# Kernel tuning notes

Hardware: AMD Instinct MI355X
Metric: run time of the kernel (lower is better)

The kernel has to match this reference:

```python
import jax, jax.numpy as jnp
import numpy as np
from jax.ops import segment_sum

N_GRAPHS, N_PER = 100, 1000
N = N_GRAPHS * N_PER
DEG = 32
E = N * DEG
RATIO = 0.8
K = int(np.ceil(RATIO * N_PER))  # 800, equal-size graphs -> fixed k
F_IN, F_MID, F_OUT = 128, 16, 256


def setup_inputs() -> dict:
    key = jax.random.key(0)
    ks = jax.random.split(key, 10)
    x = jax.random.normal(ks[0], (N, F_IN), dtype=jnp.float32)
    # intra-graph random edges
    epg = E // N_GRAPHS
    src_l = jax.random.randint(ks[1], (N_GRAPHS, epg), 0, N_PER)
    dst_l = jax.random.randint(ks[2], (N_GRAPHS, epg), 0, N_PER)
    offs = (jnp.arange(N_GRAPHS) * N_PER)[:, None]
    edge_index = jnp.stack([(src_l + offs).reshape(-1), (dst_l + offs).reshape(-1)]).astype(jnp.int32)
    batch = jnp.repeat(jnp.arange(N_GRAPHS, dtype=jnp.int32), N_PER)
    s = lambda fan: 1.0 / np.sqrt(fan)
    W1 = jax.random.normal(ks[3], (F_IN, F_MID), dtype=jnp.float32) * s(F_IN)
    b1 = jnp.zeros((F_MID,), dtype=jnp.float32)
    w_rel = jax.random.normal(ks[4], (F_MID, 1), dtype=jnp.float32) * s(F_MID)
    b_rel = jnp.zeros((1,), dtype=jnp.float32)
    w_root = jax.random.normal(ks[5], (F_MID, 1), dtype=jnp.float32) * s(F_MID)
    W2 = jax.random.normal(ks[6], (F_MID, F_OUT), dtype=jnp.float32) * s(F_MID)
    b2 = jnp.zeros((F_OUT,), dtype=jnp.float32)
    return {"x": x, "edge_index": edge_index, "batch": batch,
            "W1": W1, "b1": b1, "w_rel": w_rel, "b_rel": b_rel,
            "w_root": w_root, "W2": W2, "b2": b2}


def _gcn(x, src, dst, W, b, self_w, ew, n):
    # GCNConv with self-loops: D^{-1/2}(A+I)D^{-1/2} X W + b; masked variant
    deg = segment_sum(ew, dst, num_segments=n) + self_w
    dis = jnp.where(deg > 0, jax.lax.rsqrt(deg), 0.0)
    xw = x @ W
    coef = ew * dis[src] * dis[dst]                       # [E]
    agg = segment_sum(xw[src] * coef[:, None], dst, num_segments=n)
    agg = agg + xw * (self_w * dis * dis)[:, None]        # self-loop term
    return agg + b


def reference(x, edge_index, batch, W1, b1, w_rel, b_rel, w_root, W2, b2):
    src, dst = edge_index[0], edge_index[1]
    ones_n = jnp.ones((N,), dtype=x.dtype)
    ones_e = jnp.ones((src.shape[0],), dtype=x.dtype)
    # conv1 + relu
    h = jax.nn.relu(_gcn(x, src, dst, W1, b1, ones_n, ones_e, N))
    # SAGPooling score: GraphConv(16,1) -> tanh
    agg = segment_sum(h[src], dst, num_segments=N)
    score = jnp.tanh((agg @ w_rel + h @ w_root + b_rel)[:, 0])  # [N]
    # per-graph top-k (equal graph sizes -> fixed K), expressed as node mask
    sc2 = score.reshape(N_GRAPHS, N_PER)
    _, idx = jax.lax.top_k(sc2, K)
    mask = jnp.zeros((N_GRAPHS, N_PER), dtype=x.dtype)
    mask = mask.at[jnp.arange(N_GRAPHS)[:, None], idx].set(1.0).reshape(-1)  # [N]
    h = h * (score * mask)[:, None]                       # x[perm] * score[perm]
    em = mask[src] * mask[dst]                            # filter_adj as edge mask
    # conv2 + relu on surviving nodes only
    h2 = jax.nn.relu(_gcn(h, src, dst, W2, b2, mask, em, N)) * mask[:, None]
    # global mean pool over surviving nodes per graph
    sums = segment_sum(h2, batch, num_segments=N_GRAPHS)
    cnt = segment_sum(mask, batch, num_segments=N_GRAPHS)
    return sums / cnt[:, None]
```

## Files before the change

kernel.cpp:

```cpp
#include <hip/hip_runtime.h>
#include <math.h>

#define N_NODES 100000
#define NG 100
#define N_PER 1000
#define N_EDGES 3200000
#define EPG 32000
#define EPG4 8000
#define EPGP 35008
#define K_TOP 800
#define F_IN 128
#define F_MID 16
#define F_OUT 256
#define SENT 1000
#define NCH 8
#define CHN 128

typedef __attribute__((ext_vector_type(8))) short short8;
typedef __attribute__((ext_vector_type(4))) float floatx4;

__device__ __forceinline__ unsigned short f2bf(float x) {
    union { float f; unsigned int u; } c; c.f = x;
    unsigned int u = c.u;
    u = u + 0x7FFF + ((u >> 16) & 1);
    return (unsigned short)(u >> 16);
}
__device__ __forceinline__ void add4(float4& a, const float4 b) {
    a.x += b.x; a.y += b.y; a.z += b.z; a.w += b.w;
}
__device__ __forceinline__ unsigned int fkey(float f) {
    unsigned int u = __float_as_uint(f);
    return (u & 0x80000000u) ? ~u : (u | 0x80000000u);
}

__global__ __launch_bounds__(1024) void k_front(const float* __restrict__ x,
    const float* __restrict__ W1, const int* __restrict__ ei,
    unsigned short* __restrict__ csr, int* __restrict__ crG,
    float* __restrict__ dis1G, float* __restrict__ xw1)
{
    int b = blockIdx.x, t = threadIdx.x;
    if (b < NG) {
        __shared__ int cnts[N_PER];
        __shared__ int cur[N_PER];
        __shared__ int rs[N_PER];
        __shared__ int scan[1024];
        int g = b, ebase = g * EPG, nbase = g * N_PER;
        if (b == 0 && t < F_MID) xw1[(size_t)N_NODES * F_MID + t] = 0.f;
        const int4* dst4 = (const int4*)(ei + N_EDGES + ebase);
        const int4* src4 = (const int4*)(ei + ebase);
        if (t < N_PER) { cnts[t] = 0; cur[t] = 0; }
        __syncthreads();
        for (int i = t; i < EPG4; i += 1024) {
            int4 d = dst4[i];
            atomicAdd(&cnts[d.x - nbase], 1);
            atomicAdd(&cnts[d.y - nbase], 1);
            atomicAdd(&cnts[d.z - nbase], 1);
            atomicAdd(&cnts[d.w - nbase], 1);
        }
        __syncthreads();
        int c = (t < N_PER) ? cnts[t] : 0;
        int c4 = (c + 3) & ~3;
        scan[t] = c4;
        __syncthreads();
        for (int dd = 1; dd < 1024; dd <<= 1) {
            int v = (t >= dd) ? scan[t - dd] : 0;
            __syncthreads();
            scan[t] += v;
            __syncthreads();
        }
        int exc = scan[t] - c4;
        unsigned short* cg = csr + (size_t)g * EPGP;
        if (t < N_PER) {
            rs[t] = exc;
            crG[nbase + t] = (c << 16) | exc;
            dis1G[nbase + t] = rsqrtf((float)c + 1.0f);
            for (int q = c; q < c4; q++) cg[exc + q] = (unsigned short)SENT;
        }
        __syncthreads();
        for (int i = t; i < EPG4; i += 1024) {
            int4 d = dst4[i];
            int4 s = src4[i];
            int dl, p;
            dl = d.x - nbase; p = rs[dl] + atomicAdd(&cur[dl], 1); cg[p] = (unsigned short)(s.x - nbase);
            dl = d.y - nbase; p = rs[dl] + atomicAdd(&cur[dl], 1); cg[p] = (unsigned short)(s.y - nbase);
            dl = d.z - nbase; p = rs[dl] + atomicAdd(&cur[dl], 1); cg[p] = (unsigned short)(s.z - nbase);
            dl = d.w - nbase; p = rs[dl] + atomicAdd(&cur[dl], 1); cg[p] = (unsigned short)(s.w - nbase);
        }
    } else {
        int n = (b - NG) * 1024 + t;
        if (n >= N_NODES) return;
        const float4* xr = (const float4*)(x + (size_t)n * F_IN);
        float4 a0 = {0,0,0,0}, a1 = a0, a2 = a0, a3 = a0;
#pragma unroll 4
        for (int kk = 0; kk < 32; kk++) {
            float4 xv = xr[kk];
#pragma unroll
            for (int r = 0; r < 4; r++) {
                const float4* wr = (const float4*)(W1 + (kk * 4 + r) * F_MID);
                float xs = (r == 0) ? xv.x : (r == 1) ? xv.y : (r == 2) ? xv.z : xv.w;
                float4 w0 = wr[0], w1 = wr[1], w2 = wr[2], w3 = wr[3];
                a0.x = fmaf(xs, w0.x, a0.x); a0.y = fmaf(xs, w0.y, a0.y);
                a0.z = fmaf(xs, w0.z, a0.z); a0.w = fmaf(xs, w0.w, a0.w);
                a1.x = fmaf(xs, w1.x, a1.x); a1.y = fmaf(xs, w1.y, a1.y);
                a1.z = fmaf(xs, w1.z, a1.z); a1.w = fmaf(xs, w1.w, a1.w);
                a2.x = fmaf(xs, w2.x, a2.x); a2.y = fmaf(xs, w2.y, a2.y);
                a2.z = fmaf(xs, w2.z, a2.z); a2.w = fmaf(xs, w2.w, a2.w);
                a3.x = fmaf(xs, w3.x, a3.x); a3.y = fmaf(xs, w3.y, a3.y);
                a3.z = fmaf(xs, w3.z, a3.z); a3.w = fmaf(xs, w3.w, a3.w);
            }
        }
        float4* op = (float4*)(xw1 + (size_t)n * F_MID);
        op[0] = a0; op[1] = a1; op[2] = a2; op[3] = a3;
    }
}

__global__ __launch_bounds__(512) void k_conv1(const unsigned short* __restrict__ csr,
    const int* __restrict__ crG,
    const float* __restrict__ dis1G, const float* __restrict__ xw1,
    const float* __restrict__ b1, const float* __restrict__ w_rel,
    const float* __restrict__ w_root,
    float* __restrict__ hG, float* __restrict__ hwG, float* __restrict__ hroG)
{
    __shared__ float dis1l[N_PER + 1];
    int t = threadIdx.x, b = blockIdx.x;
    int g = b % NG, chunk = b / NG;
    int nbase = g * N_PER;
    const unsigned short* cg = csr + (size_t)g * EPGP;
    if (b == 0 && t < F_MID) hG[(size_t)N_NODES * F_MID + t] = 0.f;
    for (int i = t; i < N_PER; i += 512) dis1l[i] = dis1G[nbase + i];
    if (t == 0) dis1l[SENT] = 0.f;
    __syncthreads();

    int grp = t >> 2, l = t & 3;
    int n = chunk * CHN + grp;
    if (n >= N_PER) return;
    int cr = crG[nbase + n];
    int c4 = ((cr >> 16) + 3) & ~3;
    const unsigned short* cp = cg + (cr & 0xFFFF);
    float4 a0 = {0,0,0,0}, a1 = a0, a2 = a0, a3 = a0;
    for (int k = 0; k < c4; k += 4) {
        uint2 wv = *(const uint2*)(cp + k);
        int s0 = wv.x & 0xFFFF, s1 = wv.x >> 16, s2 = wv.y & 0xFFFF, s3 = wv.y >> 16;
        float4 v0 = *(const float4*)(xw1 + ((size_t)(nbase + s0) << 4) + 4 * l);
        float4 v1 = *(const float4*)(xw1 + ((size_t)(nbase + s1) << 4) + 4 * l);
        float4 v2 = *(const float4*)(xw1 + ((size_t)(nbase + s2) << 4) + 4 * l);
        float4 v3 = *(const float4*)(xw1 + ((size_t)(nbase + s3) << 4) + 4 * l);
        float w0 = dis1l[s0], w1 = dis1l[s1], w2 = dis1l[s2], w3 = dis1l[s3];
        a0.x = fmaf(v0.x, w0, a0.x); a0.y = fmaf(v0.y, w0, a0.y); a0.z = fmaf(v0.z, w0, a0.z); a0.w = fmaf(v0.w, w0, a0.w);
        a1.x = fmaf(v1.x, w1, a1.x); a1.y = fmaf(v1.y, w1, a1.y); a1.z = fmaf(v1.z, w1, a1.z); a1.w = fmaf(v1.w, w1, a1.w);
        a2.x = fmaf(v2.x, w2, a2.x); a2.y = fmaf(v2.y, w2, a2.y); a2.z = fmaf(v2.z, w2, a2.z); a2.w = fmaf(v2.w, w2, a2.w);
        a3.x = fmaf(v3.x, w3, a3.x); a3.y = fmaf(v3.y, w3, a3.y); a3.z = fmaf(v3.z, w3, a3.z); a3.w = fmaf(v3.w, w3, a3.w);
    }
    add4(a0, a1); add4(a2, a3); add4(a0, a2);
    float dn = dis1l[n];
    float4 sfr = *(const float4*)(xw1 + ((size_t)(nbase + n) << 4) + 4 * l);
    float4 b14 = *(const float4*)(b1 + 4 * l);
    float4 hv;
    hv.x = fmaxf(fmaf(dn, fmaf(sfr.x, dn, a0.x), b14.x), 0.f);
    hv.y = fmaxf(fmaf(dn, fmaf(sfr.y, dn, a0.y), b14.y), 0.f);
    hv.z = fmaxf(fmaf(dn, fmaf(sfr.z, dn, a0.z), b14.z), 0.f);
    hv.w = fmaxf(fmaf(dn, fmaf(sfr.w, dn, a0.w), b14.w), 0.f);
    *(float4*)(hG + ((size_t)(nbase + n) << 4) + 4 * l) = hv;

    float4 wr4 = *(const float4*)(w_rel + 4 * l);
    float4 wo4 = *(const float4*)(w_root + 4 * l);
    float p1 = hv.x * wr4.x + hv.y * wr4.y + hv.z * wr4.z + hv.w * wr4.w;
    float p2 = hv.x * wo4.x + hv.y * wo4.y + hv.z * wo4.z + hv.w * wo4.w;
    p1 += __shfl_xor(p1, 1); p1 += __shfl_xor(p1, 2);
    p2 += __shfl_xor(p2, 1); p2 += __shfl_xor(p2, 2);
    if (l == 0) { hwG[nbase + n] = p1; hroG[nbase + n] = p2; }
}

__global__ __launch_bounds__(1024) void k_mid(const unsigned short* __restrict__ csr,
    const int* __restrict__ crG,
    const float* __restrict__ hwG, const float* __restrict__ hroG,
    const float* __restrict__ b_rel,
    float* __restrict__ mskG, float* __restrict__ dis2G, float* __restrict__ wsrcG,
    float* __restrict__ out)
{
    __shared__ float hwl[N_PER + 1];
    __shared__ float sc[N_PER];
    __shared__ float msk[N_PER + 1];
    __shared__ int cntl[N_PER];
    __shared__ int rsl[N_PER];
    __shared__ int hist[1024];
    __shared__ int sh_b1, sh_r1, sh_b2, sh_r2, sh_len, sh_cntgt;
    __shared__ float sh_thr;

    int t = threadIdx.x, g = blockIdx.x;
    int nbase = g * N_PER;
    const unsigned short* cg = csr + (size_t)g * EPGP;
    int grp = t >> 2, l = t & 3;

    if (t < N_PER) {
        int cr = crG[nbase + t];
        cntl[t] = cr >> 16; rsl[t] = cr & 0xFFFF;
        hwl[t] = hwG[nbase + t];
    }
    if (t == 0) { sh_cntgt = 0; sh_len = 0; hwl[SENT] = 0.f; }
    if (t < F_OUT) out[g * F_OUT + t] = 0.f;
    float brel = b_rel[0];
    __syncthreads();

#pragma unroll
    for (int rr = 0; rr < 4; rr++) {
        int n = grp + 256 * rr;
        if (n < N_PER) {
            int c4 = (cntl[n] + 3) & ~3;
            const unsigned short* cp = cg + rsl[n];
            float sm = 0.f;
            for (int k = 0; k < c4; k += 4) {
                uint2 wv = *(const uint2*)(cp + k);
                int s = (l == 0) ? (int)(wv.x & 0xFFFF) : (l == 1) ? (int)(wv.x >> 16)
                      : (l == 2) ? (int)(wv.y & 0xFFFF) : (int)(wv.y >> 16);
                sm += hwl[s];
            }
            sm += __shfl_xor(sm, 1); sm += __shfl_xor(sm, 2);
            if (l == 0) sc[n] = tanhf(sm + hroG[nbase + n] + brel);
        }
    }
    __syncthreads();

    unsigned int mykey = (t < N_PER) ? fkey(sc[t]) : 0u;
    hist[t] = 0;
    __syncthreads();
    if (t < N_PER) atomicAdd(&hist[mykey >> 22], 1);
    __syncthreads();
    {
        int v0 = hist[t]; __syncthreads();
        hist[1023 - t] = v0; __syncthreads();
        for (int dd = 1; dd < 1024; dd <<= 1) {
            int v = (t >= dd) ? hist[t - dd] : 0;
            __syncthreads(); hist[t] += v; __syncthreads();
        }
        int Sb = hist[1023 - t];
        int Snext = (t == 1023) ? 0 : hist[1022 - t];
        if (Sb >= K_TOP && Snext < K_TOP) { sh_b1 = t; sh_r1 = K_TOP - Snext; }
    }
    __syncthreads();
    int b1v = sh_b1, r1 = sh_r1;
    hist[t] = 0;
    __syncthreads();
    if (t < N_PER && (int)(mykey >> 22) == b1v) atomicAdd(&hist[(mykey >> 12) & 1023], 1);
    __syncthreads();
    {
        int v0 = hist[t]; __syncthreads();
        hist[1023 - t] = v0; __syncthreads();
        for (int dd = 1; dd < 1024; dd <<= 1) {
            int v = (t >= dd) ? hist[t - dd] : 0;
            __syncthreads(); hist[t] += v; __syncthreads();
        }
        int Sb = hist[1023 - t];
        int Snext = (t == 1023) ? 0 : hist[1022 - t];
        if (Sb >= r1 && Snext < r1) { sh_b2 = t; sh_r2 = r1 - Snext; }
    }
    __syncthreads();
    unsigned int pref = ((unsigned int)b1v << 10) | (unsigned int)sh_b2;
    int r2 = sh_r2;
    __syncthreads();
    if (t < N_PER && (mykey >> 12) == pref) { int p = atomicAdd(&sh_len, 1); hist[p] = (int)mykey; }
    __syncthreads();
    {
        int L = sh_len;
        if (t < L) {
            unsigned int k0 = (unsigned int)hist[t];
            int gcnt = 0, ecnt = 0;
            for (int q2 = 0; q2 < L; q2++) {
                unsigned int kq = (unsigned int)hist[q2];
                gcnt += (kq > k0); ecnt += (kq == k0);
            }
            if (gcnt < r2 && r2 <= gcnt + ecnt)
                sh_thr = __uint_as_float((k0 & 0x80000000u) ? (k0 & 0x7FFFFFFFu) : ~k0);
        }
    }
    __syncthreads();
    float thr = sh_thr;

    {
        bool pred = (t < N_PER) && (sc[t] > thr);
        unsigned long long bal = __ballot(pred);
        if ((t & 63) == 0) atomicAdd(&sh_cntgt, (int)__popcll(bal));
    }
    __syncthreads();
    {
        int need = K_TOP - sh_cntgt;
        if (t < N_PER) {
            float v = sc[t];
            float mm;
            if (v > thr) mm = 1.f;
            else if (v < thr) mm = 0.f;
            else {
                int r = 0;
                for (int q2 = 0; q2 < t; q2++) if (sc[q2] == thr) r++;
                mm = (r < need) ? 1.f : 0.f;
            }
            msk[t] = mm;
        }
        if (t == 0) msk[SENT] = 0.f;
    }
    __syncthreads();

#pragma unroll
    for (int rr = 0; rr < 4; rr++) {
        int n = grp + 256 * rr;
        if (n < N_PER) {
            int c4 = (cntl[n] + 3) & ~3;
            const unsigned short* cp = cg + rsl[n];
            float sm = 0.f;
            for (int k = 0; k < c4; k += 4) {
                uint2 wv = *(const uint2*)(cp + k);
                int s = (l == 0) ? (int)(wv.x & 0xFFFF) : (l == 1) ? (int)(wv.x >> 16)
                      : (l == 2) ? (int)(wv.y & 0xFFFF) : (int)(wv.y >> 16);
                sm += msk[s];
            }
            sm += __shfl_xor(sm, 1); sm += __shfl_xor(sm, 2);
            if (l == 0) {
                float d2 = msk[n] * (sm + 1.f);
                float di = (d2 > 0.f) ? rsqrtf(d2) : 0.f;
                mskG[nbase + n] = msk[n];
                dis2G[nbase + n] = di;
                wsrcG[nbase + n] = sc[n] * msk[n] * di;
            }
        }
    }
}

__global__ __launch_bounds__(512) void k_conv2(const unsigned short* __restrict__ csr,
    const int* __restrict__ crG,
    const float* __restrict__ hG, const float* __restrict__ wsrcG,
    const float* __restrict__ dis2G, const float* __restrict__ mskG,
    const float* __restrict__ W2, const float* __restrict__ b2,
    float* __restrict__ out)
{
    __shared__ float wsrcl[N_PER + 1];
    __shared__ __align__(16) unsigned short fbf[CHN * F_MID];
    __shared__ __align__(16) unsigned short w2t[F_OUT * F_MID];
    __shared__ float mskl[CHN];
    int t = threadIdx.x, b = blockIdx.x;
    int g = b % NG, chunk = b / NG;
    int nbase = g * N_PER, n0 = chunk * CHN;
    const unsigned short* cg = csr + (size_t)g * EPGP;

    for (int i = t; i < N_PER; i += 512) wsrcl[i] = wsrcG[nbase + i];
    if (t == 0) wsrcl[SENT] = 0.f;
    for (int i = t; i < F_OUT * F_MID; i += 512) {
        int f = i >> 4, jj = i & 15;
        w2t[i] = f2bf(W2[jj * F_OUT + f]);
    }
    __syncthreads();

    int grp = t >> 2, l = t & 3;
    int n = n0 + grp;
    if (n < N_PER) {
        float di = dis2G[nbase + n];
        float4 pv = {0.f, 0.f, 0.f, 0.f};
        if (di != 0.f) {
            int cr = crG[nbase + n];
            int c4 = ((cr >> 16) + 3) & ~3;
            const unsigned short* cp = cg + (cr & 0xFFFF);
            float4 a0 = {0,0,0,0}, a1 = a0, a2 = a0, a3 = a0;
            for (int k = 0; k < c4; k += 4) {
                uint2 wv = *(const uint2*)(cp + k);
                int s0 = wv.x & 0xFFFF, s1 = wv.x >> 16, s2 = wv.y & 0xFFFF, s3 = wv.y >> 16;
                float4 v0 = *(const float4*)(hG + ((size_t)(nbase + s0) << 4) + 4 * l);
                float4 v1 = *(const float4*)(hG + ((size_t)(nbase + s1) << 4) + 4 * l);
                float4 v2 = *(const float4*)(hG + ((size_t)(nbase + s2) << 4) + 4 * l);
                float4 v3 = *(const float4*)(hG + ((size_t)(nbase + s3) << 4) + 4 * l);
                float w0 = wsrcl[s0], w1 = wsrcl[s1], w2 = wsrcl[s2], w3 = wsrcl[s3];
                a0.x = fmaf(v0.x, w0, a0.x); a0.y = fmaf(v0.y, w0, a0.y); a0.z = fmaf(v0.z, w0, a0.z); a0.w = fmaf(v0.w, w0, a0.w);
                a1.x = fmaf(v1.x, w1, a1.x); a1.y = fmaf(v1.y, w1, a1.y); a1.z = fmaf(v1.z, w1, a1.z); a1.w = fmaf(v1.w, w1, a1.w);
                a2.x = fmaf(v2.x, w2, a2.x); a2.y = fmaf(v2.y, w2, a2.y); a2.z = fmaf(v2.z, w2, a2.z); a2.w = fmaf(v2.w, w2, a2.w);
                a3.x = fmaf(v3.x, w3, a3.x); a3.y = fmaf(v3.y, w3, a3.y); a3.z = fmaf(v3.z, w3, a3.z); a3.w = fmaf(v3.w, w3, a3.w);
            }
            add4(a0, a1); add4(a2, a3); add4(a0, a2);
            float wn = wsrcl[n];
            float4 hs = *(const float4*)(hG + ((size_t)(nbase + n) << 4) + 4 * l);
            pv.x = di * fmaf(hs.x, wn, a0.x);
            pv.y = di * fmaf(hs.y, wn, a0.y);
            pv.z = di * fmaf(hs.z, wn, a0.z);
            pv.w = di * fmaf(hs.w, wn, a0.w);
        }
        unsigned int pk0 = (unsigned int)f2bf(pv.x) | ((unsigned int)f2bf(pv.y) << 16);
        unsigned int pk1 = (unsigned int)f2bf(pv.z) | ((unsigned int)f2bf(pv.w) << 16);
        *(unsigned int*)(fbf + grp * F_MID + 4 * l) = pk0;
        *(unsigned int*)(fbf + grp * F_MID + 4 * l + 2) = pk1;
        if (l == 0) mskl[grp] = mskG[nbase + n];
    } else {
        *(unsigned int*)(fbf + grp * F_MID + 4 * l) = 0u;
        *(unsigned int*)(fbf + grp * F_MID + 4 * l + 2) = 0u;
        if (l == 0) mskl[grp] = 0.f;
    }
    __syncthreads();

    {
        int wave = t >> 6, lane = t & 63;
        int q = lane >> 4, fl = lane & 15;
        int c0 = 32 * wave + fl, c1 = c0 + 16;
        float b2f0 = b2[c0], b2f1 = b2[c1];
        short8 bfrag0 = {0,0,0,0,0,0,0,0}, bfrag1 = bfrag0;
        if (q < 2) {
            bfrag0 = *(const short8*)(w2t + c0 * F_MID + q * 8);
            bfrag1 = *(const short8*)(w2t + c1 * F_MID + q * 8);
        }
        floatx4 zero = {0.f, 0.f, 0.f, 0.f};
        float acc0 = 0.f, acc1 = 0.f;
        for (int tile = 0; tile < CHN / 16; tile++) {
            short8 afrag = {0,0,0,0,0,0,0,0};
            int na = tile * 16 + fl;
            if (q < 2)
                afrag = *(const short8*)(fbf + na * F_MID + q * 8);
            floatx4 d0 = __builtin_amdgcn_mfma_f32_16x16x32_bf16(afrag, bfrag0, zero, 0, 0, 0);
            floatx4 d1 = __builtin_amdgcn_mfma_f32_16x16x32_bf16(afrag, bfrag1, zero, 0, 0, 0);
#pragma unroll
            for (int r = 0; r < 4; r++) {
                int nd = tile * 16 + q * 4 + r;
                float m = mskl[nd];
                acc0 += m * fmaxf(d0[r] + b2f0, 0.f);
                acc1 += m * fmaxf(d1[r] + b2f1, 0.f);
            }
        }
        acc0 += __shfl_xor(acc0, 16); acc0 += __shfl_xor(acc0, 32);
        acc1 += __shfl_xor(acc1, 16); acc1 += __shfl_xor(acc1, 32);
        if (lane < 16) {
            atomicAdd(&out[g * F_OUT + c0], acc0 * (1.0f / (float)K_TOP));
            atomicAdd(&out[g * F_OUT + c1], acc1 * (1.0f / (float)K_TOP));
        }
    }
}

extern "C" void kernel_launch(void* const* d_in, const int* in_sizes, int n_in,
                              void* d_out, int out_size, void* d_ws, size_t ws_size,
                              hipStream_t stream) {
    const float* x      = (const float*)d_in[0];
    const int*   ei     = (const int*)d_in[1];
    const float* W1     = (const float*)d_in[3];
    const float* b1     = (const float*)d_in[4];
    const float* w_rel  = (const float*)d_in[5];
    const float* b_rel  = (const float*)d_in[6];
    const float* w_root = (const float*)d_in[7];
    const float* W2     = (const float*)d_in[8];
    const float* b2     = (const float*)d_in[9];
    float* out = (float*)d_out;

    char* ws = (char*)d_ws;
    size_t o = 0;
    auto nxt = [&](size_t bytes) { void* p = ws + o; o += (bytes + 255) & ~(size_t)255; return p; };
    unsigned short* csr = (unsigned short*)nxt((size_t)NG * EPGP * sizeof(unsigned short));
    int*   crG   = (int*)nxt((size_t)N_NODES * sizeof(int));
    float* dis1G = (float*)nxt((size_t)N_NODES * sizeof(float));
    float* xw1   = (float*)nxt(((size_t)N_NODES + 1) * F_MID * sizeof(float));
    float* hG    = (float*)nxt(((size_t)N_NODES + 1) * F_MID * sizeof(float));
    float* hwG   = (float*)nxt((size_t)N_NODES * sizeof(float));
    float* hroG  = (float*)nxt((size_t)N_NODES * sizeof(float));
    float* mskG  = (float*)nxt((size_t)N_NODES * sizeof(float));
    float* dis2G = (float*)nxt((size_t)N_NODES * sizeof(float));
    float* wsrcG = (float*)nxt((size_t)N_NODES * sizeof(float));

    int gemm_blocks = (N_NODES + 1023) / 1024;
    k_front<<<NG + gemm_blocks, 1024, 0, stream>>>(x, W1, ei, csr, crG, dis1G, xw1);
    k_conv1<<<NG * NCH, 512, 0, stream>>>(csr, crG, dis1G, xw1, b1, w_rel, w_root, hG, hwG, hroG);
    k_mid<<<NG, 1024, 0, stream>>>(csr, crG, hwG, hroG, b_rel, mskG, dis2G, wsrcG, out);
    k_conv2<<<NG * NCH, 512, 0, stream>>>(csr, crG, hG, wsrcG, dis2G, mskG, W2, b2, out);
}
```

Measured before the change: 234.7 us.

## Build per-graph CSR in shared memory using saved atomic ranks, then copy out

The CSR construction in the front kernel now keeps the slot index returned by the counting atomics, packed four 8-bit ranks per edge quad in shared memory. The scatter pass then needs no second set of atomics. The whole per-graph CSR is assembled in shared memory and written to global memory with coalesced 16-byte stores, replacing scattered 2-byte global writes. This raises shared memory use to roughly 120 KB per block, which may limit occupancy. The 8-bit ranks assume each destination has in-degree of at most 255.

New measurement: 224.7 us. -4.3%, faster.

```diff
diff --git a/kernel.cpp b/kernel.cpp
--- a/kernel.cpp
+++ b/kernel.cpp
@@ -38,24 +38,27 @@
     unsigned short* __restrict__ csr, int* __restrict__ crG,
     float* __restrict__ dis1G, float* __restrict__ xw1)
 {
+    __shared__ int cnts[N_PER];
+    __shared__ int rs[N_PER];
+    __shared__ int scan[1024];
+    __shared__ unsigned int rank4[EPG4];
+    __shared__ __align__(16) unsigned short csrl[EPGP];
+
     int b = blockIdx.x, t = threadIdx.x;
     if (b < NG) {
-        __shared__ int cnts[N_PER];
-        __shared__ int cur[N_PER];
-        __shared__ int rs[N_PER];
-        __shared__ int scan[1024];
         int g = b, ebase = g * EPG, nbase = g * N_PER;
         if (b == 0 && t < F_MID) xw1[(size_t)N_NODES * F_MID + t] = 0.f;
         const int4* dst4 = (const int4*)(ei + N_EDGES + ebase);
         const int4* src4 = (const int4*)(ei + ebase);
-        if (t < N_PER) { cnts[t] = 0; cur[t] = 0; }
+        if (t < N_PER) cnts[t] = 0;
         __syncthreads();
         for (int i = t; i < EPG4; i += 1024) {
             int4 d = dst4[i];
-            atomicAdd(&cnts[d.x - nbase], 1);
-            atomicAdd(&cnts[d.y - nbase], 1);
-            atomicAdd(&cnts[d.z - nbase], 1);
-            atomicAdd(&cnts[d.w - nbase], 1);
+            unsigned r0 = (unsigned)atomicAdd(&cnts[d.x - nbase], 1);
+            unsigned r1 = (unsigned)atomicAdd(&cnts[d.y - nbase], 1);
+            unsigned r2 = (unsigned)atomicAdd(&cnts[d.z - nbase], 1);
+            unsigned r3 = (unsigned)atomicAdd(&cnts[d.w - nbase], 1);
+            rank4[i] = r0 | (r1 << 8) | (r2 << 16) | (r3 << 24);
         }
         __syncthreads();
         int c = (t < N_PER) ? cnts[t] : 0;
@@ -69,22 +72,27 @@
             __syncthreads();
         }
         int exc = scan[t] - c4;
-        unsigned short* cg = csr + (size_t)g * EPGP;
         if (t < N_PER) {
             rs[t] = exc;
             crG[nbase + t] = (c << 16) | exc;
             dis1G[nbase + t] = rsqrtf((float)c + 1.0f);
-            for (int q = c; q < c4; q++) cg[exc + q] = (unsigned short)SENT;
+            for (int q = c; q < c4; q++) csrl[exc + q] = (unsigned short)SENT;
         }
         __syncthreads();
         for (int i = t; i < EPG4; i += 1024) {
             int4 d = dst4[i];
             int4 s = src4[i];
-            int dl, p;
-            dl = d.x - nbase; p = rs[dl] + atomicAdd(&cur[dl], 1); cg[p] = (unsigned short)(s.x - nbase);
-            dl = d.y - nbase; p = rs[dl] + atomicAdd(&cur[dl], 1); cg[p] = (unsigned short)(s.y - nbase);
-            dl = d.z - nbase; p = rs[dl] + atomicAdd(&cur[dl], 1); cg[p] = (unsigned short)(s.z - nbase);
-            dl = d.w - nbase; p = rs[dl] + atomicAdd(&cur[dl], 1); cg[p] = (unsigned short)(s.w - nbase);
+            unsigned rk = rank4[i];
+            csrl[rs[d.x - nbase] + (rk & 255u)]         = (unsigned short)(s.x - nbase);
+            csrl[rs[d.y - nbase] + ((rk >> 8) & 255u)]  = (unsigned short)(s.y - nbase);
+            csrl[rs[d.z - nbase] + ((rk >> 16) & 255u)] = (unsigned short)(s.z - nbase);
+            csrl[rs[d.w - nbase] + (rk >> 24)]          = (unsigned short)(s.w - nbase);
+        }
+        __syncthreads();
+        {
+            const uint4* sv = (const uint4*)csrl;
+            uint4* dv = (uint4*)(csr + (size_t)g * EPGP);
+            for (int i = t; i < EPGP / 8; i += 1024) dv[i] = sv[i];
         }
     } else {
         int n = (b - NG) * 1024 + t;
```
